# Performance work log

Measured on AMD Instinct MI355X. Metric: run time of the kernel, lower is better.

Reference implementation:

```python
import jax, jax.numpy as jnp
import numpy as np

BATCH = 524288

# --- spiking gate primitives on {0,1} floats (differentiable polynomial forms) ---
def AND(a, b): return a * b
def OR(a, b): return a + b - a * b
def XOR(a, b): return a + b - 2.0 * a * b
def NOT(a): return 1.0 - a
def MUX(s, a, b): return s * a + (1.0 - s) * b  # s==1 -> a

def or_tree(x):
    return 1.0 - jnp.prod(1.0 - x, axis=-1, keepdims=True)

def and_tree(x):
    return jnp.prod(x, axis=-1, keepdims=True)

def comparator(a, b):
    # MSB-first unsigned compare; returns (a_gt_b, a_eq_b), each [...,1]
    eq = 1.0 - XOR(a, b)
    pre = jnp.cumprod(eq, axis=-1)
    pre_excl = jnp.concatenate([jnp.ones_like(pre[..., :1]), pre[..., :-1]], axis=-1)
    gt_bits = a * (1.0 - b) * pre_excl
    a_gt = 1.0 - jnp.prod(1.0 - gt_bits, axis=-1, keepdims=True)
    return a_gt, pre[..., -1:]

def add_lsb(a, b):
    # ripple-carry adder, LSB-first bits; returns (sum_lsb, carry_out[...,1])
    a_t = jnp.moveaxis(a, -1, 0)
    b_t = jnp.moveaxis(b, -1, 0)
    def step(c, ab):
        ai, bi = ab
        s = XOR(XOR(ai, bi), c)
        c2 = OR(AND(ai, bi), AND(c, XOR(ai, bi)))
        return c2, s
    c0 = jnp.zeros(a.shape[:-1], a.dtype)
    c, s = jax.lax.scan(step, c0, (a_t, b_t))
    return jnp.moveaxis(s, 0, -1), c[..., None]

def sub_lsb(a, b):
    # ripple-borrow subtractor a-b, LSB-first; returns (diff_lsb, borrow_out)
    a_t = jnp.moveaxis(a, -1, 0)
    b_t = jnp.moveaxis(b, -1, 0)
    def step(bor, ab):
        ai, bi = ab
        d = XOR(XOR(ai, bi), bor)
        bor2 = OR(AND(NOT(ai), OR(bi, bor)), AND(bi, bor))
        return bor2, d
    b0 = jnp.zeros(a.shape[:-1], a.dtype)
    bor, d = jax.lax.scan(step, b0, (a_t, b_t))
    return jnp.moveaxis(d, 0, -1), bor[..., None]

def barrel_right_sticky(m, amt):
    # m: [...,28] MSB-first; amt: [...,5] MSB-first (weights 16,8,4,2,1)
    sticky = jnp.zeros(m.shape[:-1] + (1,), m.dtype)
    for i, k in enumerate((16, 8, 4, 2, 1)):
        s = amt[..., i:i + 1]
        shifted = jnp.concatenate([jnp.zeros_like(m[..., :k]), m[..., :-k]], axis=-1)
        sticky = OR(sticky, AND(s, or_tree(m[..., -k:])))
        m = MUX(s, shifted, m)
    return m, sticky

def barrel_left(m, amt):
    for i, k in enumerate((16, 8, 4, 2, 1)):
        s = amt[..., i:i + 1]
        shifted = jnp.concatenate([m[..., k:], jnp.zeros_like(m[..., :k])], axis=-1)
        m = MUX(s, shifted, m)
    return m

def _bits5(v):
    return [float((v >> s) & 1) for s in (4, 3, 2, 1, 0)]

_LZC_CODES = np.array([_bits5(i) for i in range(28)], dtype=np.float32)  # [28,5] MSB-first
_LZC_28 = np.array(_bits5(28), dtype=np.float32)

def lzd28(m):
    # leading-zero count of 28-bit MSB-first word as 5-bit MSB-first code
    nz_pre = jnp.cumprod(1.0 - m, axis=-1)
    pre_excl = jnp.concatenate([jnp.ones_like(nz_pre[..., :1]), nz_pre[..., :-1]], axis=-1)
    first_one = m * pre_excl  # one-hot position of leading 1
    all_zero = nz_pre[..., -1:]
    return first_one @ jnp.asarray(_LZC_CODES) + all_zero * jnp.asarray(_LZC_28)

def fp32_add(A, B):
    bshape = A.shape[:-1]
    z1 = jnp.zeros(bshape + (1,), A.dtype)
    o1 = jnp.ones(bshape + (1,), A.dtype)
    s_a, e_a, m_a_raw = A[..., 0:1], A[..., 1:9], A[..., 9:32]
    s_b, e_b, m_b_raw = B[..., 0:1], B[..., 1:9], B[..., 9:32]

    e_a_nonzero = or_tree(e_a); hidden_a = e_a_nonzero
    e_b_nonzero = or_tree(e_b); hidden_b = e_b_nonzero
    e_one = jnp.concatenate([z1] * 7 + [o1], axis=-1)
    e_a_eff = MUX(NOT(e_a_nonzero), e_one, e_a)
    e_b_eff = MUX(NOT(e_b_nonzero), e_one, e_b)
    z4 = jnp.zeros(bshape + (4,), A.dtype)
    m_a = jnp.concatenate([hidden_a, m_a_raw, z4], axis=-1)  # 28-bit mantissa
    m_b = jnp.concatenate([hidden_b, m_b_raw, z4], axis=-1)

    a_exp_gt, a_exp_eq = comparator(e_a_eff, e_b_eff)
    a_mant_gt, a_mant_eq = comparator(jnp.concatenate([hidden_a, m_a_raw], -1),
                                      jnp.concatenate([hidden_b, m_b_raw], -1))
    a_abs_eq_b = AND(a_exp_eq, a_mant_eq)
    a_ge_b = OR(a_exp_gt, AND(a_exp_eq, OR(a_mant_gt, a_mant_eq)))

    diff_ab_lsb, _ = sub_lsb(jnp.flip(e_a_eff, -1), jnp.flip(e_b_eff, -1))
    diff_ba_lsb, _ = sub_lsb(jnp.flip(e_b_eff, -1), jnp.flip(e_a_eff, -1))
    exp_diff = MUX(a_ge_b, jnp.flip(diff_ab_lsb, -1), jnp.flip(diff_ba_lsb, -1))

    is_big_diff = OR(or_tree(exp_diff[..., 0:3]), AND(exp_diff[..., 3:4], exp_diff[..., 4:5]))  # diff>=24
    shift_amt = exp_diff[..., 3:8]

    e_max = MUX(a_ge_b, e_a_eff, e_b_eff)
    m_large = MUX(a_ge_b, m_a, m_b)
    m_small_uns = MUX(a_ge_b, m_b, m_a)
    m_small, shift_sticky = barrel_right_sticky(m_small_uns, shift_amt)
    # big exponent difference: small operand contributes only to sticky
    m_small = MUX(is_big_diff, jnp.zeros_like(m_small), m_small)
    shift_sticky = MUX(is_big_diff, or_tree(m_small_uns), shift_sticky)

    is_diff_sign = XOR(s_a, s_b)
    exact_cancel = AND(is_diff_sign, a_abs_eq_b)
    s_large = MUX(a_ge_b, s_a, s_b)

    ml_lsb = jnp.flip(m_large, -1)
    ms_lsb = jnp.flip(m_small, -1)
    sum_lsb, sum_carry = add_lsb(ml_lsb, ms_lsb)
    diff_lsb, _ = sub_lsb(ml_lsb, ms_lsb)
    sum_result = jnp.flip(sum_lsb, -1)
    diff_result = jnp.flip(diff_lsb, -1)

    need_sub_one = AND(is_diff_sign, shift_sticky)
    one28_lsb = jnp.concatenate([o1] + [z1] * 27, axis=-1)
    dm1_lsb, _ = sub_lsb(diff_lsb, one28_lsb)
    diff_final = MUX(need_sub_one, jnp.flip(dm1_lsb, -1), diff_result)

    mant_res = MUX(is_diff_sign, diff_final, sum_result)
    result_carry = MUX(is_diff_sign, z1, sum_carry)

    lzc = lzd28(mant_res)
    lzc8 = jnp.concatenate([z1, z1, z1, lzc], axis=-1)
    u_gt, u_eq = comparator(lzc8, e_max)
    is_underflow = OR(u_gt, u_eq)

    norm_mant = barrel_left(mant_res, lzc)
    ean_lsb, _ = sub_lsb(jnp.flip(e_max, -1), jnp.flip(lzc8, -1))
    e_after_norm = jnp.flip(ean_lsb, -1)
    one8 = jnp.concatenate([z1] * 7 + [o1], axis=-1)
    ep1_lsb, _ = add_lsb(jnp.flip(e_max, -1), jnp.flip(one8, -1))
    e_plus_one = jnp.flip(ep1_lsb, -1)
    zero8 = jnp.zeros(bshape + (8,), A.dtype)
    e_normal = MUX(is_underflow, zero8, e_after_norm)
    final_e_pre = MUX(result_carry, e_plus_one, e_normal)

    m_overflow = mant_res[..., 0:23]
    round_overflow = mant_res[..., 23:24]
    sticky_overflow = or_tree(mant_res[..., 24:28])
    m_norm = norm_mant[..., 1:24]
    round_norm = norm_mant[..., 24:25]
    sticky_norm = or_tree(norm_mant[..., 25:28])
    m_subnorm = mant_res[..., 0:23]

    m_pre = MUX(result_carry, m_overflow, m_norm)
    round_pre = MUX(result_carry, round_overflow, round_norm)
    sticky_pre = OR(MUX(result_carry, sticky_overflow, sticky_norm), shift_sticky)
    m_sel = MUX(is_underflow, m_subnorm, m_pre)

    L = m_sel[..., 22:23]
    do_round = AND(AND(round_pre, OR(sticky_pre, L)), NOT(is_underflow))

    msel_lsb = jnp.flip(m_sel, -1)
    m24_lsb = jnp.concatenate([msel_lsb, z1], axis=-1)
    inc = jnp.concatenate([do_round] + [z1] * 23, axis=-1)
    mr_lsb, _ = add_lsb(m24_lsb, inc)
    round_carry = mr_lsb[..., 23:24]  # mantissa overflow after rounding
    m_rounded = jnp.flip(mr_lsb[..., :23], -1)
    m_final = AND(NOT(round_carry), m_rounded)
    er_inc = jnp.concatenate([z1] * 7 + [round_carry], axis=-1)
    er_lsb, _ = add_lsb(jnp.flip(final_e_pre, -1), jnp.flip(er_inc, -1))
    computed_e = MUX(round_carry, jnp.flip(er_lsb, -1), final_e_pre)

    cancel_s = MUX(exact_cancel, z1, s_large)
    cancel_e = MUX(exact_cancel, zero8, computed_e)
    cancel_m = MUX(exact_cancel, jnp.zeros_like(m_final), m_final)

    e_a_all1 = and_tree(e_a); m_a_nz = or_tree(m_a_raw)
    e_b_all1 = and_tree(e_b); m_b_nz = or_tree(m_b_raw)
    any_nan = OR(AND(e_a_all1, m_a_nz), AND(e_b_all1, m_b_nz))
    a_is_inf = AND(e_a_all1, NOT(m_a_nz))
    b_is_inf = AND(e_b_all1, NOT(m_b_nz))
    any_inf = OR(a_is_inf, b_is_inf)
    result_is_nan = OR(any_nan, AND(is_diff_sign, AND(a_is_inf, b_is_inf)))

    ones8 = jnp.ones_like(e_a)
    nan_res = jnp.concatenate([z1, ones8, jnp.ones_like(m_a_raw)], axis=-1)
    inf_res = jnp.concatenate([s_large, ones8, jnp.zeros_like(m_a_raw)], axis=-1)

    overflow = and_tree(computed_e)  # exponent saturated -> +/-Inf
    normal = jnp.concatenate([cancel_s, cancel_e, cancel_m], axis=-1)
    out = MUX(OR(any_inf, overflow), inf_res, normal)
    out = MUX(result_is_nan, nan_res, out)
    return out

def setup_inputs():
    key = jax.random.key(0)
    kA, kB = jax.random.split(key)
    A = jax.random.randint(kA, (BATCH, 32), 0, 2).astype(jnp.float32)
    B = jax.random.randint(kB, (BATCH, 32), 0, 2).astype(jnp.float32)
    return {"A": A, "B": B}

def reference(A, B):
    return fp32_add(A, B)
```

## Files before the change

### kernel.cpp

```cpp
#include <hip/hip_runtime.h>
#include <stdint.h>

typedef float    f32x4 __attribute__((ext_vector_type(4)));
typedef uint32_t u32x4 __attribute__((ext_vector_type(4)));

__device__ __forceinline__ uint32_t soft_fp32_add(uint32_t aw, uint32_t bw) {
    const uint32_t M28 = 0x0FFFFFFFu;
    uint32_t sa = aw >> 31, sb = bw >> 31;
    uint32_t ea = (aw >> 23) & 0xFFu, eb = (bw >> 23) & 0xFFu;
    uint32_t ma = aw & 0x7FFFFFu,     mb = bw & 0x7FFFFFu;
    uint32_t ha = (ea != 0u) ? 1u : 0u, hb = (eb != 0u) ? 1u : 0u;
    uint32_t eaf = ha ? ea : 1u;
    uint32_t ebf = hb ? eb : 1u;
    uint32_t mA = (ha << 27) | (ma << 4);
    uint32_t mB = (hb << 27) | (mb << 4);
    uint32_t keyA = (eaf << 24) | (ha << 23) | ma;
    uint32_t keyB = (ebf << 24) | (hb << 23) | mb;
    uint32_t age  = (keyA >= keyB) ? 1u : 0u;
    uint32_t abeq = (keyA == keyB) ? 1u : 0u;
    uint32_t ediff = age ? (eaf - ebf) : (ebf - eaf);
    uint32_t big = (ediff >= 24u) ? 1u : 0u;
    uint32_t sh  = ediff & 31u;
    uint32_t emax = age ? eaf : ebf;
    uint32_t ml   = age ? mA : mB;
    uint32_t msu  = age ? mB : mA;
    uint32_t ms     = msu >> sh;
    uint32_t sticky = ((msu & ((1u << sh) - 1u)) != 0u) ? 1u : 0u;
    if (big) { ms = 0u; sticky = (msu != 0u) ? 1u : 0u; }
    uint32_t dsgn   = sa ^ sb;
    uint32_t cancel = dsgn & abeq;
    uint32_t sl     = age ? sa : sb;
    uint32_t sum    = ml + ms;
    uint32_t scarry = sum >> 28;
    uint32_t sres   = sum & M28;
    uint32_t diff   = (ml - ms) & M28;
    uint32_t dfin   = (dsgn & sticky) ? ((diff - 1u) & M28) : diff;
    uint32_t mant   = dsgn ? dfin : sres;
    uint32_t rc     = dsgn ? 0u : scarry;
    uint32_t lzc    = mant ? (uint32_t)(__clz((int)mant) - 4) : 28u;
    uint32_t undf   = (lzc >= emax) ? 1u : 0u;
    uint32_t norm   = (mant << lzc) & M28;
    uint32_t e_aft  = (emax - lzc) & 0xFFu;
    uint32_t e_p1   = (emax + 1u) & 0xFFu;
    uint32_t e_nrm  = undf ? 0u : e_aft;
    uint32_t fe     = rc ? e_p1 : e_nrm;
    uint32_t m_ovf  = mant >> 5;
    uint32_t r_ovf  = (mant >> 4) & 1u;
    uint32_t st_ovf = ((mant & 0xFu) != 0u) ? 1u : 0u;
    uint32_t m_nrm  = (norm >> 4) & 0x7FFFFFu;
    uint32_t r_nrm  = (norm >> 3) & 1u;
    uint32_t st_nrm = ((norm & 7u) != 0u) ? 1u : 0u;
    uint32_t m_pre  = rc ? m_ovf : m_nrm;
    uint32_t r_pre  = rc ? r_ovf : r_nrm;
    uint32_t st_pre = (rc ? st_ovf : st_nrm) | sticky;
    uint32_t m_sel  = undf ? m_ovf : m_pre;
    uint32_t Lb     = m_sel & 1u;
    uint32_t dor    = r_pre & (st_pre | Lb) & (undf ^ 1u);
    uint32_t mr     = m_sel + dor;
    uint32_t rcar   = mr >> 23;
    uint32_t m_fin  = mr & 0x7FFFFFu;
    uint32_t ce     = (fe + rcar) & 0xFFu;
    uint32_t os = cancel ? 0u : sl;
    uint32_t oe = cancel ? 0u : ce;
    uint32_t om = cancel ? 0u : m_fin;
    uint32_t ea1 = (ea == 0xFFu) ? 1u : 0u, eb1 = (eb == 0xFFu) ? 1u : 0u;
    uint32_t manz = (ma != 0u) ? 1u : 0u, mbnz = (mb != 0u) ? 1u : 0u;
    uint32_t anynan = (ea1 & manz) | (eb1 & mbnz);
    uint32_t ainf = ea1 & (manz ^ 1u);
    uint32_t binf = eb1 & (mbnz ^ 1u);
    uint32_t anyinf = ainf | binf;
    uint32_t isnan  = anynan | (dsgn & ainf & binf);
    uint32_t ovf    = (ce == 0xFFu) ? 1u : 0u;
    uint32_t out = (os << 31) | (oe << 23) | om;
    if (anyinf | ovf) out = (sl << 31) | (0xFFu << 23);
    if (isnan)        out = (0xFFu << 23) | 0x7FFFFFu;
    return out;
}

__global__ __launch_bounds__(256) void SpikeFP32Adder_kernel(
    const uint32_t* __restrict__ A, const uint32_t* __restrict__ B,
    float* __restrict__ O, int nrows)
{
    const int t = threadIdx.x;
    const size_t rowIdx = (size_t)blockIdx.x * 256 + t;
    const size_t row = rowIdx < (size_t)nrows ? rowIdx : (size_t)nrows - 1;

    const u32x4* Arow = (const u32x4*)(A + row * 32);
    const u32x4* Brow = (const u32x4*)(B + row * 32);

    u32x4 a[8], b[8];
    #pragma unroll
    for (int j = 0; j < 8; ++j) a[j] = Arow[j];
    #pragma unroll
    for (int j = 0; j < 8; ++j) b[j] = Brow[j];

    uint32_t aw = 0u, bw = 0u;
    #pragma unroll
    for (int j = 0; j < 8; ++j) {
        const int s = 31 - 4 * j;
        aw |= ((a[j].x >> 23) & 1u) << s;
        aw |= ((a[j].y >> 23) & 1u) << (s - 1);
        aw |= ((a[j].z >> 23) & 1u) << (s - 2);
        aw |= ((a[j].w >> 23) & 1u) << (s - 3);
        bw |= ((b[j].x >> 23) & 1u) << s;
        bw |= ((b[j].y >> 23) & 1u) << (s - 1);
        bw |= ((b[j].z >> 23) & 1u) << (s - 2);
        bw |= ((b[j].w >> 23) & 1u) << (s - 3);
    }

    uint32_t outw = soft_fp32_add(aw, bw);

    __shared__ uint32_t w_lds[256];
    w_lds[t] = outw;
    __syncthreads();

    const size_t chunkBase = (size_t)blockIdx.x * 8192;
    const size_t total = (size_t)nrows * 32;
    #pragma unroll
    for (int it = 0; it < 8; ++it) {
        uint32_t w = w_lds[it * 32 + (t >> 3)];
        const int c = 4 * (t & 7);
        f32x4 f;
        f.x = (float)((w >> (31 - c)) & 1u);
        f.y = (float)((w >> (30 - c)) & 1u);
        f.z = (float)((w >> (29 - c)) & 1u);
        f.w = (float)((w >> (28 - c)) & 1u);
        size_t idx = chunkBase + (size_t)it * 1024 + 4 * (size_t)t;
        if (idx + 3 < total)
            __builtin_nontemporal_store(f, (f32x4*)(O + idx));
    }
}

extern "C" void kernel_launch(void* const* d_in, const int* in_sizes, int n_in,
                              void* d_out, int out_size, void* d_ws, size_t ws_size,
                              hipStream_t stream) {
    const uint32_t* A = (const uint32_t*)d_in[0];
    const uint32_t* B = (const uint32_t*)d_in[1];
    float* O = (float*)d_out;
    int nrows = in_sizes[0] / 32;
    int blocks = (nrows + 255) / 256;
    SpikeFP32Adder_kernel<<<dim3(blocks), dim3(256), 0, stream>>>(A, B, O, nrows);
}
```

Measured before the change: 37.48 us.

## Coalesce input loads and pack row bits with cross-lane shuffles

Each thread used to load a whole 128-byte row, so adjacent lanes read addresses 128 bytes apart. Now each iteration has lanes read contiguous 16-byte chunks, and each lane packs its 4 bits into a partial word. Groups of 8 lanes OR-reduce the partials with xor-shuffles, and one lane per group keeps the assembled word. The LDS write index is permuted so the output stage still matches rows to threads. This adds 48 shuffles per thread and a different row-to-thread mapping in exchange for fully coalesced global reads.

```diff
diff --git a/kernel.cpp b/kernel.cpp
--- a/kernel.cpp
+++ b/kernel.cpp
@@ -82,44 +82,47 @@
     float* __restrict__ O, int nrows)
 {
     const int t = threadIdx.x;
-    const size_t rowIdx = (size_t)blockIdx.x * 256 + t;
-    const size_t row = rowIdx < (size_t)nrows ? rowIdx : (size_t)nrows - 1;
+    const size_t total = (size_t)nrows * 32;
+    const size_t chunkBase = (size_t)blockIdx.x * 8192;
 
-    const u32x4* Arow = (const u32x4*)(A + row * 32);
-    const u32x4* Brow = (const u32x4*)(B + row * 32);
+    const int c = 4 * (t & 7);
+    uint32_t aw = 0u, bw = 0u;
 
-    u32x4 a[8], b[8];
     #pragma unroll
-    for (int j = 0; j < 8; ++j) a[j] = Arow[j];
-    #pragma unroll
-    for (int j = 0; j < 8; ++j) b[j] = Brow[j];
+    for (int it = 0; it < 8; ++it) {
+        size_t idx = chunkBase + (size_t)it * 1024 + 4 * (size_t)t;
+        size_t i2 = (idx + 3 < total) ? idx : (total - 4);
+        u32x4 av = *(const u32x4*)(A + i2);
+        u32x4 bv = *(const u32x4*)(B + i2);
 
-    uint32_t aw = 0u, bw = 0u;
-    #pragma unroll
-    for (int j = 0; j < 8; ++j) {
-        const int s = 31 - 4 * j;
-        aw |= ((a[j].x >> 23) & 1u) << s;
-        aw |= ((a[j].y >> 23) & 1u) << (s - 1);
-        aw |= ((a[j].z >> 23) & 1u) << (s - 2);
-        aw |= ((a[j].w >> 23) & 1u) << (s - 3);
-        bw |= ((b[j].x >> 23) & 1u) << s;
-        bw |= ((b[j].y >> 23) & 1u) << (s - 1);
-        bw |= ((b[j].z >> 23) & 1u) << (s - 2);
-        bw |= ((b[j].w >> 23) & 1u) << (s - 3);
+        uint32_t pa = (((av.x >> 23) & 1u) << (31 - c))
+                    | (((av.y >> 23) & 1u) << (30 - c))
+                    | (((av.z >> 23) & 1u) << (29 - c))
+                    | (((av.w >> 23) & 1u) << (28 - c));
+        uint32_t pb = (((bv.x >> 23) & 1u) << (31 - c))
+                    | (((bv.y >> 23) & 1u) << (30 - c))
+                    | (((bv.z >> 23) & 1u) << (29 - c))
+                    | (((bv.w >> 23) & 1u) << (28 - c));
+
+        pa |= (uint32_t)__shfl_xor((int)pa, 1);
+        pa |= (uint32_t)__shfl_xor((int)pa, 2);
+        pa |= (uint32_t)__shfl_xor((int)pa, 4);
+        pb |= (uint32_t)__shfl_xor((int)pb, 1);
+        pb |= (uint32_t)__shfl_xor((int)pb, 2);
+        pb |= (uint32_t)__shfl_xor((int)pb, 4);
+
+        if ((t & 7) == it) { aw = pa; bw = pb; }
     }
 
     uint32_t outw = soft_fp32_add(aw, bw);
 
     __shared__ uint32_t w_lds[256];
-    w_lds[t] = outw;
+    w_lds[((t & 7) << 5) | (t >> 3)] = outw;
     __syncthreads();
 
-    const size_t chunkBase = (size_t)blockIdx.x * 8192;
-    const size_t total = (size_t)nrows * 32;
     #pragma unroll
     for (int it = 0; it < 8; ++it) {
         uint32_t w = w_lds[it * 32 + (t >> 3)];
-        const int c = 4 * (t & 7);
         f32x4 f;
         f.x = (float)((w >> (31 - c)) & 1u);
         f.y = (float)((w >> (30 - c)) & 1u);
```

New measurement: 34.04 us. 9.2% less time.
